# Kernel tuning notes

Hardware: AMD Instinct MI355X
Metric: run time of the kernel (lower is better)

Reference implementation:

```python
import jax, jax.numpy as jnp
import numpy as np

B, N, D, H = 4, 1024, 1024, 8
HD = D // H  # head dim = 128


def _layernorm(x, g, b, eps=1e-5):
    mu = jnp.mean(x, axis=-1, keepdims=True)
    var = jnp.mean(jnp.square(x - mu), axis=-1, keepdims=True)
    return (x - mu) * jax.lax.rsqrt(var + eps) * g + b


def setup_inputs() -> dict:
    key = jax.random.key(0)
    ks = jax.random.split(key, 8)
    x = jax.random.normal(ks[0], (B, N, D), dtype=jnp.float32)
    adj = (jax.random.uniform(ks[1], (B, N, N)) < 0.02).astype(jnp.int32)
    adj = jnp.maximum(adj, jnp.eye(N, dtype=jnp.int32)[None])  # self-loops: no empty softmax rows
    stoich = jax.random.normal(ks[2], (B, N), dtype=jnp.float32)
    s = 0.02
    W1 = jax.random.normal(ks[3], (D, 4 * D), dtype=jnp.float32) * s
    W2 = jax.random.normal(ks[4], (4 * D, D), dtype=jnp.float32) * s
    gW = jax.random.normal(ks[5], (D,), dtype=jnp.float32) * s  # Linear(1, D) weight
    return {
        "x": x, "adj_matrix": adj, "stoichiometry": stoich,
        "ln1_g": jnp.ones((D,), jnp.float32), "ln1_b": jnp.zeros((D,), jnp.float32),
        "ln2_g": jnp.ones((D,), jnp.float32), "ln2_b": jnp.zeros((D,), jnp.float32),
        "W1": W1, "b1": jnp.zeros((4 * D,), jnp.float32),
        "W2": W2, "b2": jnp.zeros((D,), jnp.float32),
        "gW": gW, "gb": jnp.zeros((D,), jnp.float32),
    }


def reference(x, adj_matrix, stoichiometry, ln1_g, ln1_b, ln2_g, ln2_b, W1, b1, W2, b2, gW, gb):
    normed = _layernorm(x, ln1_g, ln1_b)
    # q = k = v = normed, split into heads: [B, H, N, HD]
    qkv = normed.reshape(B, N, H, HD).transpose(0, 2, 1, 3)
    scores = jnp.einsum("bhqd,bhkd->bhqk", qkv, qkv) / jnp.sqrt(jnp.float32(HD))
    # stoichiometry gate: Linear(1, D) + sigmoid -> [B, N, D]; broadcast as [B, 1, N, D] (D == N)
    gates = jax.nn.sigmoid(stoichiometry[:, :, None] * gW + gb)[:, None]  # [B,1,N,N]
    mask = adj_matrix[:, None] > 0  # [B,1,N,N]
    # gate only valid entries (equivalent to (-inf)*gate since gate>0), then mask
    masked = jnp.where(mask, scores * gates, -jnp.inf)
    attn = jax.nn.softmax(masked, axis=-1)
    out = jnp.einsum("bhqk,bhkd->bhqd", attn, qkv)
    out = out.transpose(0, 2, 1, 3).reshape(B, N, D)
    x = x + out
    normed2 = _layernorm(x, ln2_g, ln2_b)
    mlp = jax.nn.gelu(normed2 @ W1 + b1, approximate=False) @ W2 + b2
    return x + mlp
```

## Files before the change

### kernel.cpp

```cpp
#include <hip/hip_runtime.h>
#include <math.h>

#define NTOK 1024
#define DMODEL 1024
#define NHEAD 8
#define HDIM 128
#define BATCH 4

typedef __bf16 bf16x8 __attribute__((ext_vector_type(8)));
typedef float  f32x4  __attribute__((ext_vector_type(4)));
typedef unsigned short ushort_t;
typedef unsigned short us8 __attribute__((ext_vector_type(8)));

static __device__ __forceinline__ ushort_t f2bf(float f) {
  unsigned u = __float_as_uint(f);
  u += 0x7fffu + ((u >> 16) & 1u);
  return (ushort_t)(u >> 16);
}
static __device__ __forceinline__ float bf2f(ushort_t v) {
  return __uint_as_float(((unsigned)v) << 16);
}

static __device__ __forceinline__ float fast_gelu(float v) {
  const float u = 1.5957691216057308f * (v + 0.044715f * v * v * v);
  return v / (1.f + __expf(-u));
}

static __device__ __forceinline__ void gld16(void* lds, const void* g) {
  __builtin_amdgcn_global_load_lds(
      (const __attribute__((address_space(1))) void*)g,
      (__attribute__((address_space(3))) void*)lds, 16, 0, 0);
}

__global__ __launch_bounds__(256) void prep_kernel(
    const float* __restrict__ x, const float* __restrict__ g,
    const float* __restrict__ b, ushort_t* __restrict__ out,
    const float* __restrict__ W1, ushort_t* __restrict__ W1t,
    const float* __restrict__ W2, ushort_t* __restrict__ W2t)
{
  if (blockIdx.x < 4096) {
    const int row = blockIdx.x;
    const int tid = threadIdx.x;
    const float* xr = x + (size_t)row * DMODEL;
    float4 v = *(const float4*)(xr + 4 * tid);
    float s1 = v.x + v.y + v.z + v.w;
    float s2 = v.x * v.x + v.y * v.y + v.z * v.z + v.w * v.w;
#pragma unroll
    for (int d = 1; d < 64; d <<= 1) { s1 += __shfl_xor(s1, d); s2 += __shfl_xor(s2, d); }
    __shared__ float red[10];
    const int wid = tid >> 6;
    if ((tid & 63) == 0) { red[wid] = s1; red[4 + wid] = s2; }
    __syncthreads();
    if (tid == 0) {
      float a = red[0] + red[1] + red[2] + red[3];
      float c = red[4] + red[5] + red[6] + red[7];
      float mu = a / (float)DMODEL;
      float var = c / (float)DMODEL - mu * mu;
      red[8] = mu; red[9] = rsqrtf(var + 1e-5f);
    }
    __syncthreads();
    const float mu = red[8], inv = red[9];
    float4 gg = *(const float4*)(g + 4 * tid);
    float4 bb = *(const float4*)(b + 4 * tid);
    ushort4 o;
    o.x = f2bf((v.x - mu) * inv * gg.x + bb.x);
    o.y = f2bf((v.y - mu) * inv * gg.y + bb.y);
    o.z = f2bf((v.z - mu) * inv * gg.z + bb.z);
    o.w = f2bf((v.w - mu) * inv * gg.w + bb.w);
    *(ushort4*)(out + (size_t)row * DMODEL + 4 * tid) = o;
  } else {
    __shared__ float t[32][33];
    int id = blockIdx.x - 4096;
    const float* W; ushort_t* Wt; int K, N, bx, by;
    if (id < 4096) { W = W1; Wt = W1t; K = 1024; N = 4096; bx = id & 127; by = id >> 7; }
    else { id -= 4096; W = W2; Wt = W2t; K = 4096; N = 1024; bx = id & 31; by = id >> 5; }
    const int kb = by * 32, nb = bx * 32;
    const int c = threadIdx.x & 31, r0 = threadIdx.x >> 5;
#pragma unroll
    for (int r = r0; r < 32; r += 8)
      t[r][c] = W[(size_t)(kb + r) * N + nb + c];
    __syncthreads();
#pragma unroll
    for (int r = r0; r < 32; r += 8)
      Wt[(size_t)(nb + r) * K + kb + c] = f2bf(t[c][r]);
  }
}

__global__ __launch_bounds__(256) void attn_kernel(
    const float* __restrict__ x, const ushort_t* __restrict__ normedB,
    const int* __restrict__ adj, const float* __restrict__ stoich,
    const float* __restrict__ gW, const float* __restrict__ gb,
    const float* __restrict__ ln2g, const float* __restrict__ ln2b,
    const float* __restrict__ b2,
    float* __restrict__ outbase, ushort_t* __restrict__ normed2)
{
  __shared__ int   neigh[2][NTOK];
  __shared__ float gateS[2][NTOK];
  __shared__ int   cntS[2];
  __shared__ float red[2][6];

  const int tid = threadIdx.x;
  const int sub = tid >> 7;
  const int t   = tid & 127;
  const int row = blockIdx.x * 2 + sub;
  const int b   = row >> 10;

  if (tid < 2) cntS[tid] = 0;
  __syncthreads();
  const int* arow = adj + (size_t)row * NTOK;
  {
    int4 a4 = ((const int4*)arow)[t];
    int k0 = 4 * t;
    if (a4.x > 0) { int p = atomicAdd(&cntS[sub], 1); neigh[sub][p] = k0; }
    if (a4.y > 0) { int p = atomicAdd(&cntS[sub], 1); neigh[sub][p] = k0 + 1; }
    if (a4.z > 0) { int p = atomicAdd(&cntS[sub], 1); neigh[sub][p] = k0 + 2; }
    if (a4.w > 0) { int p = atomicAdd(&cntS[sub], 1); neigh[sub][p] = k0 + 3; }
    a4 = ((const int4*)arow)[t + 128];
    k0 = 4 * (t + 128);
    if (a4.x > 0) { int p = atomicAdd(&cntS[sub], 1); neigh[sub][p] = k0; }
    if (a4.y > 0) { int p = atomicAdd(&cntS[sub], 1); neigh[sub][p] = k0 + 1; }
    if (a4.z > 0) { int p = atomicAdd(&cntS[sub], 1); neigh[sub][p] = k0 + 2; }
    if (a4.w > 0) { int p = atomicAdd(&cntS[sub], 1); neigh[sub][p] = k0 + 3; }
  }
  __syncthreads();
  const int cnt = cntS[sub];

  const float st = stoich[row];
  for (int i = t; i < cnt; i += 128) {
    int k = neigh[sub][i];
    gateS[sub][i] = 1.f / (1.f + __expf(-fmaf(st, gW[k], gb[k])));
  }
  __syncthreads();

  const ushort_t* nbB = normedB + (size_t)b * NTOK * DMODEL;
  const int d0 = 8 * t;
  us8 qu = *(const us8*)(nbB + (size_t)(row & 1023) * DMODEL + d0);
  float qv[8];
#pragma unroll
  for (int j = 0; j < 8; ++j) qv[j] = bf2f(qu[j]);
  const float scale = 0.08838834764831845f;

  float lsum = 0.f;
  float o[8] = {0.f, 0.f, 0.f, 0.f, 0.f, 0.f, 0.f, 0.f};

  for (int i0 = 0; i0 < cnt; i0 += 8) {
    us8 ku[8]; float w8[8];
#pragma unroll
    for (int u = 0; u < 8; ++u) {
      const int i = i0 + u;
      const int ii = (i < cnt) ? i : 0;
      ku[u] = *(const us8*)(nbB + (size_t)neigh[sub][ii] * DMODEL + d0);
      w8[u] = gateS[sub][ii];
    }
#pragma unroll
    for (int u = 0; u < 8; ++u) {
      float p = 0.f;
#pragma unroll
      for (int j = 0; j < 8; ++j) p = fmaf(bf2f(ku[u][j]), qv[j], p);
      p += __shfl_xor(p, 1); p += __shfl_xor(p, 2);
      p += __shfl_xor(p, 4); p += __shfl_xor(p, 8);
      w8[u] *= p * scale;
    }
#pragma unroll
    for (int u = 0; u < 8; ++u)
      w8[u] = (i0 + u < cnt) ? __expf(w8[u]) : 0.f;
#pragma unroll
    for (int u = 0; u < 8; ++u) {
      lsum += w8[u];
#pragma unroll
      for (int j = 0; j < 8; ++j) o[j] = fmaf(w8[u], bf2f(ku[u][j]), o[j]);
    }
  }
  const float pinv = 1.f / lsum;

  const float* xr = x + (size_t)row * DMODEL + d0;
  const float4 xa = *(const float4*)(xr);
  const float4 xb = *(const float4*)(xr + 4);
  float r[8];
  r[0] = xa.x + o[0] * pinv; r[1] = xa.y + o[1] * pinv;
  r[2] = xa.z + o[2] * pinv; r[3] = xa.w + o[3] * pinv;
  r[4] = xb.x + o[4] * pinv; r[5] = xb.y + o[5] * pinv;
  r[6] = xb.z + o[6] * pinv; r[7] = xb.w + o[7] * pinv;

  const float4 ba = *(const float4*)(b2 + d0);
  const float4 bbv = *(const float4*)(b2 + d0 + 4);
  float4 oa, ob;
  oa.x = r[0] + ba.x;  oa.y = r[1] + ba.y;  oa.z = r[2] + ba.z;  oa.w = r[3] + ba.w;
  ob.x = r[4] + bbv.x; ob.y = r[5] + bbv.y; ob.z = r[6] + bbv.z; ob.w = r[7] + bbv.w;
  float* obp = outbase + (size_t)row * DMODEL + d0;
  *(float4*)(obp) = oa;
  *(float4*)(obp + 4) = ob;

  float s1 = 0.f, s2 = 0.f;
#pragma unroll
  for (int j = 0; j < 8; ++j) { s1 += r[j]; s2 += r[j] * r[j]; }
#pragma unroll
  for (int d = 1; d < 64; d <<= 1) { s1 += __shfl_xor(s1, d); s2 += __shfl_xor(s2, d); }
  const int wsub = (tid >> 6) & 1;
  if ((tid & 63) == 0) { red[sub][wsub] = s1; red[sub][2 + wsub] = s2; }
  __syncthreads();
  if ((tid & 127) == 0) {
    float a = red[sub][0] + red[sub][1];
    float c = red[sub][2] + red[sub][3];
    float mu = a / (float)DMODEL;
    float var = c / (float)DMODEL - mu * mu;
    red[sub][4] = mu; red[sub][5] = rsqrtf(var + 1e-5f);
  }
  __syncthreads();
  const float mu = red[sub][4], inv = red[sub][5];
  const float4 ga = *(const float4*)(ln2g + d0);
  const float4 gbv = *(const float4*)(ln2g + d0 + 4);
  const float4 la = *(const float4*)(ln2b + d0);
  const float4 lb = *(const float4*)(ln2b + d0 + 4);
  const float gg[8] = {ga.x, ga.y, ga.z, ga.w, gbv.x, gbv.y, gbv.z, gbv.w};
  const float ll[8] = {la.x, la.y, la.z, la.w, lb.x, lb.y, lb.z, lb.w};
  us8 pk;
#pragma unroll
  for (int j = 0; j < 8; ++j) pk[j] = f2bf((r[j] - mu) * inv * gg[j] + ll[j]);
  *(us8*)(normed2 + (size_t)row * DMODEL + d0) = pk;
}

__global__ __launch_bounds__(256) void gemm_mfma_gelu(
    const ushort_t* __restrict__ A, const ushort_t* __restrict__ Bt,
    const float* __restrict__ bias, ushort_t* __restrict__ Cout,
    int M, int N, int K)
{
  __shared__ __align__(16) ushort_t As[2][128 * 32];
  __shared__ __align__(16) ushort_t Bs[2][128 * 32];

  const int id = blockIdx.x;
  const int xcd = id & 7, slot = id >> 3;
  const int bm = (xcd * 4 + (slot & 3)) * 128;
  const int bn = (slot >> 2) * 128;

  const int tid = threadIdx.x;
  const int w = tid >> 6, l = tid & 63;
  const int wm = (w >> 1) * 64, wn = (w & 1) * 64;

  const int srow = tid >> 2;
  const int kelem = (tid & 3) * 8;
  const ushort_t* Ag0 = A + (size_t)(bm + srow) * K + kelem;
  const ushort_t* Ag1 = A + (size_t)(bm + srow + 64) * K + kelem;
  const ushort_t* Bg0 = Bt + (size_t)(bn + srow) * K + kelem;
  const ushort_t* Bg1 = Bt + (size_t)(bn + srow + 64) * K + kelem;
  const int wb = w * 512;

  const int quad = l >> 4, lrow = l & 15;

  f32x4 acc[4][4] = {};

  for (int kb = 0; kb < K; kb += 64) {
    __syncthreads();
    gld16(&As[0][wb],        Ag0 + kb);
    gld16(&As[0][wb + 2048], Ag1 + kb);
    gld16(&Bs[0][wb],        Bg0 + kb);
    gld16(&Bs[0][wb + 2048], Bg1 + kb);
    gld16(&As[1][wb],        Ag0 + kb + 32);
    gld16(&As[1][wb + 2048], Ag1 + kb + 32);
    gld16(&Bs[1][wb],        Bg0 + kb + 32);
    gld16(&Bs[1][wb + 2048], Bg1 + kb + 32);
    __syncthreads();
#pragma unroll
    for (int s = 0; s < 2; ++s) {
      const ushort_t* aRd = &As[s][(wm + lrow) * 32 + quad * 8];
      const ushort_t* bRd = &Bs[s][(wn + lrow) * 32 + quad * 8];
      bf16x8 af[4], bfr[4];
#pragma unroll
      for (int i = 0; i < 4; ++i) af[i] = *(const bf16x8*)(aRd + i * 512);
#pragma unroll
      for (int j = 0; j < 4; ++j) bfr[j] = *(const bf16x8*)(bRd + j * 512);
#pragma unroll
      for (int i = 0; i < 4; ++i)
#pragma unroll
        for (int j = 0; j < 4; ++j)
          acc[i][j] = __builtin_amdgcn_mfma_f32_16x16x32_bf16(af[i], bfr[j], acc[i][j], 0, 0, 0);
    }
  }

#pragma unroll
  for (int i = 0; i < 4; ++i) {
    const int row0 = bm + wm + 16 * i + quad * 4;
#pragma unroll
    for (int j = 0; j < 4; ++j) {
      const int col = bn + wn + 16 * j + lrow;
      const float bi = bias[col];
#pragma unroll
      for (int r = 0; r < 4; ++r) {
        const int row = row0 + r;
        Cout[(size_t)row * N + col] = f2bf(fast_gelu(acc[i][j][r] + bi));
      }
    }
  }
}

__global__ __launch_bounds__(256) void gemm_mfma_splitk(
    const ushort_t* __restrict__ A, const ushort_t* __restrict__ Bt,
    float* __restrict__ Cout, int M, int N, int K, int kchunk)
{
  __shared__ __align__(16) ushort_t As[2][128 * 32];
  __shared__ __align__(16) ushort_t Bs[2][128 * 32];

  const int id = blockIdx.x;
  const int xcd = id & 7, slot = id >> 3;
  const int bm = (xcd * 4 + (slot & 3)) * 128;
  const int bn = ((slot >> 2) & 7) * 128;
  const int koff = (slot >> 5) * kchunk;

  const int tid = threadIdx.x;
  const int w = tid >> 6, l = tid & 63;
  const int wm = (w >> 1) * 64, wn = (w & 1) * 64;

  const int srow = tid >> 2;
  const int kelem = (tid & 3) * 8;
  const ushort_t* Ag0 = A + (size_t)(bm + srow) * K + koff + kelem;
  const ushort_t* Ag1 = A + (size_t)(bm + srow + 64) * K + koff + kelem;
  const ushort_t* Bg0 = Bt + (size_t)(bn + srow) * K + koff + kelem;
  const ushort_t* Bg1 = Bt + (size_t)(bn + srow + 64) * K + koff + kelem;
  const int wb = w * 512;

  const int quad = l >> 4, lrow = l & 15;

  f32x4 acc[4][4] = {};

  for (int kb = 0; kb < kchunk; kb += 64) {
    __syncthreads();
    gld16(&As[0][wb],        Ag0 + kb);
    gld16(&As[0][wb + 2048], Ag1 + kb);
    gld16(&Bs[0][wb],        Bg0 + kb);
    gld16(&Bs[0][wb + 2048], Bg1 + kb);
    gld16(&As[1][wb],        Ag0 + kb + 32);
    gld16(&As[1][wb + 2048], Ag1 + kb + 32);
    gld16(&Bs[1][wb],        Bg0 + kb + 32);
    gld16(&Bs[1][wb + 2048], Bg1 + kb + 32);
    __syncthreads();
#pragma unroll
    for (int s = 0; s < 2; ++s) {
      const ushort_t* aRd = &As[s][(wm + lrow) * 32 + quad * 8];
      const ushort_t* bRd = &Bs[s][(wn + lrow) * 32 + quad * 8];
      bf16x8 af[4], bfr[4];
#pragma unroll
      for (int i = 0; i < 4; ++i) af[i] = *(const bf16x8*)(aRd + i * 512);
#pragma unroll
      for (int j = 0; j < 4; ++j) bfr[j] = *(const bf16x8*)(bRd + j * 512);
#pragma unroll
      for (int i = 0; i < 4; ++i)
#pragma unroll
        for (int j = 0; j < 4; ++j)
          acc[i][j] = __builtin_amdgcn_mfma_f32_16x16x32_bf16(af[i], bfr[j], acc[i][j], 0, 0, 0);
    }
  }

#pragma unroll
  for (int i = 0; i < 4; ++i) {
    const int row0 = bm + wm + 16 * i + quad * 4;
#pragma unroll
    for (int j = 0; j < 4; ++j) {
      const int col = bn + wn + 16 * j + lrow;
#pragma unroll
      for (int r = 0; r < 4; ++r) {
        const int row = row0 + r;
        atomicAdd(&Cout[(size_t)row * N + col], acc[i][j][r]);
      }
    }
  }
}

extern "C" void kernel_launch(void* const* d_in, const int* in_sizes, int n_in,
                              void* d_out, int out_size, void* d_ws, size_t ws_size,
                              hipStream_t stream) {
  const float* x      = (const float*)d_in[0];
  const int*   adj    = (const int*)d_in[1];
  const float* stoich = (const float*)d_in[2];
  const float* ln1g   = (const float*)d_in[3];
  const float* ln1b   = (const float*)d_in[4];
  const float* ln2g   = (const float*)d_in[5];
  const float* ln2b   = (const float*)d_in[6];
  const float* W1     = (const float*)d_in[7];
  const float* b1     = (const float*)d_in[8];
  const float* W2     = (const float*)d_in[9];
  const float* b2     = (const float*)d_in[10];
  const float* gW     = (const float*)d_in[11];
  const float* gb     = (const float*)d_in[12];
  float* out = (float*)d_out;
  char* ws = (char*)d_ws;

  ushort_t* normedB = (ushort_t*)(ws);
  ushort_t* normed2 = (ushort_t*)(ws + (16u << 20));
  ushort_t* hidden  = (ushort_t*)(ws + (24u << 20));
  ushort_t* W1t     = (ushort_t*)(ws + (56u << 20));
  ushort_t* W2t     = (ushort_t*)(ws + (64u << 20));

  const int ROWS = BATCH * NTOK;

  prep_kernel<<<12288, 256, 0, stream>>>(x, ln1g, ln1b, normedB,
                                         W1, W1t, W2, W2t);
  attn_kernel<<<ROWS / 2, 256, 0, stream>>>(x, normedB, adj, stoich, gW, gb,
                                            ln2g, ln2b, b2, out, normed2);
  gemm_mfma_gelu<<<1024, 256, 0, stream>>>(normed2, W1t, b1, hidden,
                                           ROWS, 4096, 1024);
  gemm_mfma_splitk<<<512, 256, 0, stream>>>(hidden, W2t, out,
                                            ROWS, 1024, 4096, 2048);
}
```

Measured before the change: 275.2 us.

## Replace atomic split-K with 4-way partial buffers plus a separate reduce kernel

The second MLP GEMM previously used 2-way split-K with 512 blocks, presumably accumulating into the output with atomics. It now uses 4-way split-K with 1024 blocks that write fp32 partials to workspace, followed by a reduce kernel that adds the four partials into the output. This doubles parallelism and avoids atomics, at the cost of 64MB of extra partial-buffer traffic and an extra launch. It runs only if the workspace holds at least 136MB; otherwise the old path is used.

```diff
diff --git a/kernel.cpp b/kernel.cpp
--- a/kernel.cpp
+++ b/kernel.cpp
@@ -290,6 +290,100 @@
         Cout[(size_t)row * N + col] = f2bf(fast_gelu(acc[i][j][r] + bi));
       }
     }
+  }
+}
+
+__global__ __launch_bounds__(256) void gemm_mfma_partial(
+    const ushort_t* __restrict__ A, const ushort_t* __restrict__ Bt,
+    float* __restrict__ P, int M, int N, int K, int kchunk)
+{
+  __shared__ __align__(16) ushort_t As[2][128 * 32];
+  __shared__ __align__(16) ushort_t Bs[2][128 * 32];
+
+  const int id = blockIdx.x;
+  const int xcd = id & 7, slot = id >> 3;
+  const int bm = (xcd * 4 + (slot & 3)) * 128;
+  const int bn = ((slot >> 2) & 7) * 128;
+  const int z  = slot >> 5;
+  const int koff = z * kchunk;
+  float* __restrict__ Pz = P + (size_t)z * M * N;
+
+  const int tid = threadIdx.x;
+  const int w = tid >> 6, l = tid & 63;
+  const int wm = (w >> 1) * 64, wn = (w & 1) * 64;
+
+  const int srow = tid >> 2;
+  const int kelem = (tid & 3) * 8;
+  const ushort_t* Ag0 = A + (size_t)(bm + srow) * K + koff + kelem;
+  const ushort_t* Ag1 = A + (size_t)(bm + srow + 64) * K + koff + kelem;
+  const ushort_t* Bg0 = Bt + (size_t)(bn + srow) * K + koff + kelem;
+  const ushort_t* Bg1 = Bt + (size_t)(bn + srow + 64) * K + koff + kelem;
+  const int wb = w * 512;
+
+  const int quad = l >> 4, lrow = l & 15;
+
+  f32x4 acc[4][4] = {};
+
+  for (int kb = 0; kb < kchunk; kb += 64) {
+    __syncthreads();
+    gld16(&As[0][wb],        Ag0 + kb);
+    gld16(&As[0][wb + 2048], Ag1 + kb);
+    gld16(&Bs[0][wb],        Bg0 + kb);
+    gld16(&Bs[0][wb + 2048], Bg1 + kb);
+    gld16(&As[1][wb],        Ag0 + kb + 32);
+    gld16(&As[1][wb + 2048], Ag1 + kb + 32);
+    gld16(&Bs[1][wb],        Bg0 + kb + 32);
+    gld16(&Bs[1][wb + 2048], Bg1 + kb + 32);
+    __syncthreads();
+#pragma unroll
+    for (int s = 0; s < 2; ++s) {
+      const ushort_t* aRd = &As[s][(wm + lrow) * 32 + quad * 8];
+      const ushort_t* bRd = &Bs[s][(wn + lrow) * 32 + quad * 8];
+      bf16x8 af[4], bfr[4];
+#pragma unroll
+      for (int i = 0; i < 4; ++i) af[i] = *(const bf16x8*)(aRd + i * 512);
+#pragma unroll
+      for (int j = 0; j < 4; ++j) bfr[j] = *(const bf16x8*)(bRd + j * 512);
+#pragma unroll
+      for (int i = 0; i < 4; ++i)
+#pragma unroll
+        for (int j = 0; j < 4; ++j)
+          acc[i][j] = __builtin_amdgcn_mfma_f32_16x16x32_bf16(af[i], bfr[j], acc[i][j], 0, 0, 0);
+    }
+  }
+
+#pragma unroll
+  for (int i = 0; i < 4; ++i) {
+    const int row0 = bm + wm + 16 * i + quad * 4;
+#pragma unroll
+    for (int j = 0; j < 4; ++j) {
+      const int col = bn + wn + 16 * j + lrow;
+#pragma unroll
+      for (int r = 0; r < 4; ++r) {
+        const int row = row0 + r;
+        Pz[(size_t)row * N + col] = acc[i][j][r];
+      }
+    }
+  }
+}
+
+__global__ __launch_bounds__(256) void splitk_reduce(
+    const float* __restrict__ P, float* __restrict__ out, int nq)
+{
+  const float4* p0 = (const float4*)P;
+  const float4* p1 = p0 + nq;
+  const float4* p2 = p1 + nq;
+  const float4* p3 = p2 + nq;
+  float4* o4 = (float4*)out;
+  const int stride = gridDim.x * 256;
+  for (int i = blockIdx.x * 256 + threadIdx.x; i < nq; i += stride) {
+    float4 o = o4[i];
+    float4 a = p0[i], b = p1[i], c = p2[i], d = p3[i];
+    o.x += a.x + b.x + c.x + d.x;
+    o.y += a.y + b.y + c.y + d.y;
+    o.z += a.z + b.z + c.z + d.z;
+    o.w += a.w + b.w + c.w + d.w;
+    o4[i] = o;
   }
 }
 
@@ -389,6 +483,7 @@
   ushort_t* hidden  = (ushort_t*)(ws + (24u << 20));
   ushort_t* W1t     = (ushort_t*)(ws + (56u << 20));
   ushort_t* W2t     = (ushort_t*)(ws + (64u << 20));
+  float*    parts   = (float*)(ws + (72u << 20));
 
   const int ROWS = BATCH * NTOK;
 
@@ -398,6 +493,12 @@
                                             ln2g, ln2b, b2, out, normed2);
   gemm_mfma_gelu<<<1024, 256, 0, stream>>>(normed2, W1t, b1, hidden,
                                            ROWS, 4096, 1024);
-  gemm_mfma_splitk<<<512, 256, 0, stream>>>(hidden, W2t, out,
-                                            ROWS, 1024, 4096, 2048);
-}
+  if (ws_size >= ((size_t)136 << 20)) {
+    gemm_mfma_partial<<<1024, 256, 0, stream>>>(hidden, W2t, parts,
+                                                ROWS, 1024, 4096, 1024);
+    splitk_reduce<<<2048, 256, 0, stream>>>(parts, out, ROWS * 1024 / 4);
+  } else {
+    gemm_mfma_splitk<<<512, 256, 0, stream>>>(hidden, W2t, out,
+                                              ROWS, 1024, 4096, 2048);
+  }
+}
```

After: 287.9 us. 4.6% more time.

## Rewrite first MLP GEMM with 256x256 tiles, swizzled LDS and pipelined loads

Applied to the files above, without the earlier changes.

Replaces the 128x128-tile GELU GEMM with a 512-thread kernel that computes 256x256 output tiles over 64-wide K steps. The LDS layout is XOR-swizzled to avoid bank conflicts. Loads for the next K tile are issued in quarters between MFMA groups, using partial vmcnt waits and s_setprio to overlap global-to-LDS traffic with compute. The aim is higher arithmetic intensity and hidden memory latency. The cost is a grid of only 256 blocks, 128KB of LDS per block, and many more accumulator registers, which may limit occupancy.

```diff
diff --git a/kernel.cpp b/kernel.cpp
--- a/kernel.cpp
+++ b/kernel.cpp
@@ -3,8 +3,6 @@
 
 #define NTOK 1024
 #define DMODEL 1024
-#define NHEAD 8
-#define HDIM 128
 #define BATCH 4
 
 typedef __bf16 bf16x8 __attribute__((ext_vector_type(8)));
@@ -220,75 +218,119 @@
   *(us8*)(normed2 + (size_t)row * DMODEL + d0) = pk;
 }
 
-__global__ __launch_bounds__(256) void gemm_mfma_gelu(
+__global__ __launch_bounds__(512, 2) void gemm1_pipe(
     const ushort_t* __restrict__ A, const ushort_t* __restrict__ Bt,
     const float* __restrict__ bias, ushort_t* __restrict__ Cout,
     int M, int N, int K)
 {
-  __shared__ __align__(16) ushort_t As[2][128 * 32];
-  __shared__ __align__(16) ushort_t Bs[2][128 * 32];
+  __shared__ __align__(16) ushort_t As[2][256 * 64];
+  __shared__ __align__(16) ushort_t Bs[2][256 * 64];
 
   const int id = blockIdx.x;
   const int xcd = id & 7, slot = id >> 3;
-  const int bm = (xcd * 4 + (slot & 3)) * 128;
-  const int bn = (slot >> 2) * 128;
+  const int bm = (xcd * 2 + (slot >> 4)) * 256;
+  const int bn = (slot & 15) * 256;
 
   const int tid = threadIdx.x;
-  const int w = tid >> 6, l = tid & 63;
-  const int wm = (w >> 1) * 64, wn = (w & 1) * 64;
-
-  const int srow = tid >> 2;
-  const int kelem = (tid & 3) * 8;
-  const ushort_t* Ag0 = A + (size_t)(bm + srow) * K + kelem;
-  const ushort_t* Ag1 = A + (size_t)(bm + srow + 64) * K + kelem;
-  const ushort_t* Bg0 = Bt + (size_t)(bn + srow) * K + kelem;
-  const ushort_t* Bg1 = Bt + (size_t)(bn + srow + 64) * K + kelem;
-  const int wb = w * 512;
+  const int l = tid & 63;
+  const int wid = tid >> 6;
+  const int wrow = (wid >> 2) * 128;
+  const int wcol = (wid & 3) * 64;
+
+  const int sr = tid >> 3;
+  const int sg = tid & 7;
+  const int gsrc = ((sg ^ (sr & 7)) << 3);
+  const ushort_t* Ag = A  + (size_t)(bm + sr) * K + gsrc;
+  const ushort_t* Bg = Bt + (size_t)(bn + sr) * K + gsrc;
+  const int dst = tid * 8;
 
   const int quad = l >> 4, lrow = l & 15;
-
-  f32x4 acc[4][4] = {};
-
-  for (int kb = 0; kb < K; kb += 64) {
-    __syncthreads();
-    gld16(&As[0][wb],        Ag0 + kb);
-    gld16(&As[0][wb + 2048], Ag1 + kb);
-    gld16(&Bs[0][wb],        Bg0 + kb);
-    gld16(&Bs[0][wb + 2048], Bg1 + kb);
-    gld16(&As[1][wb],        Ag0 + kb + 32);
-    gld16(&As[1][wb + 2048], Ag1 + kb + 32);
-    gld16(&Bs[1][wb],        Bg0 + kb + 32);
-    gld16(&Bs[1][wb + 2048], Bg1 + kb + 32);
-    __syncthreads();
-#pragma unroll
-    for (int s = 0; s < 2; ++s) {
-      const ushort_t* aRd = &As[s][(wm + lrow) * 32 + quad * 8];
-      const ushort_t* bRd = &Bs[s][(wn + lrow) * 32 + quad * 8];
-      bf16x8 af[4], bfr[4];
-#pragma unroll
-      for (int i = 0; i < 4; ++i) af[i] = *(const bf16x8*)(aRd + i * 512);
-#pragma unroll
-      for (int j = 0; j < 4; ++j) bfr[j] = *(const bf16x8*)(bRd + j * 512);
-#pragma unroll
-      for (int i = 0; i < 4; ++i)
-#pragma unroll
-        for (int j = 0; j < 4; ++j)
-          acc[i][j] = __builtin_amdgcn_mfma_f32_16x16x32_bf16(af[i], bfr[j], acc[i][j], 0, 0, 0);
-    }
-  }
-
-#pragma unroll
-  for (int i = 0; i < 4; ++i) {
-    const int row0 = bm + wm + 16 * i + quad * 4;
+  const int swz = lrow & 7;
+  const int gx0 = ((quad ^ swz) << 3);
+  const int gx1 = (((quad + 4) ^ swz) << 3);
+
+  f32x4 acc[8][4] = {};
+  bf16x8 bfr[4];
+
+#define STAGE2(buf, kb, c0, MAT, PTR)                                          \
+  gld16(&MAT[buf][(c0) * 4096 + dst],       PTR + (size_t)(c0) * 64 * K + (kb)); \
+  gld16(&MAT[buf][((c0) + 1) * 4096 + dst], PTR + (size_t)((c0) + 1) * 64 * K + (kb));
+
+#define QUARTER(buf, GX, IH, LB)                                               \
+  {                                                                            \
+    if (LB) {                                                                  \
+      _Pragma("unroll")                                                        \
+      for (int j = 0; j < 4; ++j) {                                            \
+        const int rb = wcol + j * 16 + lrow;                                   \
+        bfr[j] = *(const bf16x8*)(&Bs[buf][rb * 64 + (GX)]);                   \
+      }                                                                        \
+    }                                                                          \
+    bf16x8 af[4];                                                              \
+    _Pragma("unroll")                                                          \
+    for (int ii = 0; ii < 4; ++ii) {                                           \
+      const int ra = wrow + (IH) * 64 + ii * 16 + lrow;                        \
+      af[ii] = *(const bf16x8*)(&As[buf][ra * 64 + (GX)]);                     \
+    }                                                                          \
+    __builtin_amdgcn_s_setprio(1);                                             \
+    _Pragma("unroll")                                                          \
+    for (int ii = 0; ii < 4; ++ii)                                             \
+      _Pragma("unroll")                                                        \
+      for (int j = 0; j < 4; ++j)                                              \
+        acc[(IH) * 4 + ii][j] = __builtin_amdgcn_mfma_f32_16x16x32_bf16(       \
+            af[ii], bfr[j], acc[(IH) * 4 + ii][j], 0, 0, 0);                   \
+    __builtin_amdgcn_s_setprio(0);                                             \
+  }
+
+  STAGE2(0, 0, 0, As, Ag); STAGE2(0, 0, 2, As, Ag);
+  STAGE2(0, 0, 0, Bs, Bg); STAGE2(0, 0, 2, Bs, Bg);
+  asm volatile("s_waitcnt vmcnt(0)" ::: "memory");
+  __builtin_amdgcn_s_barrier();
+
+  const int NTK = K >> 6;
+#pragma unroll 1
+  for (int t = 0; t < NTK - 1; ++t) {
+    const int cb = t & 1, nb = cb ^ 1;
+    const int kb = (t + 1) << 6;
+    STAGE2(nb, kb, 0, As, Ag);
+    __builtin_amdgcn_sched_barrier(0);
+    asm volatile("s_waitcnt vmcnt(2)" ::: "memory");
+    __builtin_amdgcn_s_barrier();
+    __builtin_amdgcn_sched_barrier(0);
+    QUARTER(cb, gx0, 0, 1);
+    __builtin_amdgcn_s_barrier();
+    STAGE2(nb, kb, 2, As, Ag);
+    QUARTER(cb, gx0, 1, 0);
+    __builtin_amdgcn_s_barrier();
+    STAGE2(nb, kb, 0, Bs, Bg);
+    QUARTER(cb, gx1, 0, 1);
+    __builtin_amdgcn_s_barrier();
+    STAGE2(nb, kb, 2, Bs, Bg);
+    QUARTER(cb, gx1, 1, 0);
+    __builtin_amdgcn_s_barrier();
+  }
+  {
+    const int cb = (NTK - 1) & 1;
+    asm volatile("s_waitcnt vmcnt(0)" ::: "memory");
+    __builtin_amdgcn_s_barrier();
+    __builtin_amdgcn_sched_barrier(0);
+    QUARTER(cb, gx0, 0, 1);
+    QUARTER(cb, gx0, 1, 0);
+    QUARTER(cb, gx1, 0, 1);
+    QUARTER(cb, gx1, 1, 0);
+  }
+#undef STAGE2
+#undef QUARTER
+
+#pragma unroll
+  for (int i = 0; i < 8; ++i) {
+    const int row0 = bm + wrow + 16 * i + quad * 4;
 #pragma unroll
     for (int j = 0; j < 4; ++j) {
-      const int col = bn + wn + 16 * j + lrow;
+      const int col = bn + wcol + 16 * j + lrow;
       const float bi = bias[col];
 #pragma unroll
-      for (int r = 0; r < 4; ++r) {
-        const int row = row0 + r;
-        Cout[(size_t)row * N + col] = f2bf(fast_gelu(acc[i][j][r] + bi));
-      }
+      for (int r = 0; r < 4; ++r)
+        Cout[(size_t)(row0 + r) * N + col] = f2bf(fast_gelu(acc[i][j][r] + bi));
     }
   }
 }
@@ -396,8 +438,8 @@
                                          W1, W1t, W2, W2t);
   attn_kernel<<<ROWS / 2, 256, 0, stream>>>(x, normedB, adj, stoich, gW, gb,
                                             ln2g, ln2b, b2, out, normed2);
-  gemm_mfma_gelu<<<1024, 256, 0, stream>>>(normed2, W1t, b1, hidden,
-                                           ROWS, 4096, 1024);
+  gemm1_pipe<<<256, 512, 0, stream>>>(normed2, W1t, b1, hidden,
+                                      ROWS, 4096, 1024);
   gemm_mfma_splitk<<<512, 256, 0, stream>>>(hidden, W2t, out,
                                             ROWS, 1024, 4096, 2048);
 }
```

Result: no change. 276.1 us (+0.3%).
